# Optimization experiments

Measured on AMD Instinct MI355X. Metric: run time of the kernel, lower is better.

The kernel has to match this reference:

```python
import jax, jax.numpy as jnp
import numpy as np

OUTPUT_LEN = 128

def setup_inputs() -> dict:
    key = jax.random.key(0)
    k1, k2, k3 = jax.random.split(key, 3)
    B, D = 256, 1024
    scale = 1.0 / np.sqrt(D)
    x = jax.random.normal(k1, (B, D), dtype=jnp.float32)
    W = jax.random.normal(k2, (D, 3 * D), dtype=jnp.float32) * scale  # input kernel [d, 3d] (z|r|h)
    U = jax.random.normal(k3, (D, 3 * D), dtype=jnp.float32) * scale  # recurrent kernel [d, 3d]
    b = jnp.zeros((3 * D,), dtype=jnp.float32)
    return {"x": x, "W": W, "U": U, "b": b}

def _gru_cell(inp, h, W, U, b):
    # Classic GRU (reset_after=False), Keras gate order z, r, h and
    # update rule h_new = z * h + (1 - z) * hh.
    gx = inp @ W + b              # [B, 3d]
    gh = h @ U                    # [B, 3d]
    xz, xr, xh = jnp.split(gx, 3, axis=-1)
    hz, hr, hh_lin = jnp.split(gh, 3, axis=-1)
    z = jax.nn.sigmoid(xz + hz)
    r = jax.nn.sigmoid(xr + hr)
    hh = jnp.tanh(xh + r * hh_lin)
    return z * h + (1.0 - z) * hh

def reference(x, W, U, b):
    # x: [B, d] is the initial GRU state; the first step's input is zeros,
    # afterwards each step's output (== new state) is fed back as input.
    def step(carry, _):
        inp, h = carry
        new_h = _gru_cell(inp, h, W, U, b)
        return (new_h, new_h), new_h

    init = (jnp.zeros_like(x), x)
    _, outs = jax.lax.scan(step, init, None, length=OUTPUT_LEN)  # [T, B, d]
    return jnp.transpose(outs, (1, 0, 2))  # [B, T, d]
```

## Files before the change

### kernel.cpp

```cpp
#include <hip/hip_runtime.h>
#include <stdint.h>

#define B_ROWS 256
#define DDIM   1024
#define TSTEPS 128
#define THREE_D 3072

typedef short bf16x8 __attribute__((ext_vector_type(8)));
typedef float f32x4  __attribute__((ext_vector_type(4)));
typedef unsigned short u16x8 __attribute__((ext_vector_type(8)));

static __device__ __forceinline__ unsigned short f2bf(float f) {
    union { float f; uint32_t u; } v; v.f = f;
    uint32_t u = v.u;
    uint32_t r = u + 0x7FFFu + ((u >> 16) & 1u);
    return (unsigned short)(r >> 16);
}
static __device__ __forceinline__ float bf2f(unsigned short h) {
    union { uint32_t u; float f; } v; v.u = ((uint32_t)h) << 16; return v.f;
}

__global__ __launch_bounds__(256) void pack_kernel(
    const float* __restrict__ W, const float* __restrict__ U,
    unsigned short* __restrict__ phi, unsigned short* __restrict__ plo)
{
    int t = blockIdx.x * 256 + threadIdx.x;
    int lane  = t & 63;
    int ktile = (t >> 6) & 31;
    int ntile = t >> 11;
    int col = ntile * 16 + (lane & 15);
    int q = col >> 10;
    int d = col & 1023;
    int k8 = ktile * 32 + ((lane >> 4) << 3);

    u16x8 ohi, olo;
    #pragma unroll
    for (int j = 0; j < 8; ++j) {
        int k = k8 + j;
        const float* wr = W + (size_t)k * THREE_D;
        const float* ur = U + (size_t)k * THREE_D;
        float v;
        if (q == 0)      v = wr[d] + ur[d];
        else if (q == 1) v = wr[1024 + d] + ur[1024 + d];
        else if (q == 2) v = wr[2048 + d];
        else             v = ur[2048 + d];
        unsigned short hi = f2bf(v);
        ohi[j] = hi;
        olo[j] = f2bf(v - bf2f(hi));
    }
    size_t base = ((size_t)(ntile * 32 + ktile) * 64 + lane) * 8;
    *(u16x8*)(phi + base) = ohi;
    *(u16x8*)(plo + base) = olo;
}

__global__ __launch_bounds__(256) void gru_step0(
    const float* __restrict__ x, const float* __restrict__ U,
    const float* __restrict__ bias,
    float* __restrict__ out,
    unsigned short* __restrict__ hbh, unsigned short* __restrict__ hbl)
{
    __shared__ float xt[16][64];
    const int tid = threadIdx.x;
    const int c   = tid & 63;
    const int rg  = tid >> 6;
    const int dt  = blockIdx.x & 15;
    const int rt  = blockIdx.x >> 4;

    float acc[4][3];
    #pragma unroll
    for (int rr = 0; rr < 4; ++rr) { acc[rr][0] = 0.f; acc[rr][1] = 0.f; acc[rr][2] = 0.f; }

    for (int kc = 0; kc < 16; ++kc) {
        #pragma unroll
        for (int i = 0; i < 4; ++i) {
            int e = i * 256 + tid;
            int row = e >> 6, kk = e & 63;
            xt[row][kk] = x[(size_t)(rt * 16 + row) * DDIM + kc * 64 + kk];
        }
        __syncthreads();
        #pragma unroll 4
        for (int kk = 0; kk < 64; ++kk) {
            int k = kc * 64 + kk;
            const float* up = U + (size_t)k * THREE_D + dt * 64 + c;
            float uz = up[0], ur = up[1024], uh = up[2048];
            #pragma unroll
            for (int rr = 0; rr < 4; ++rr) {
                float xv = xt[rg * 4 + rr][kk];
                acc[rr][0] += xv * uz;
                acc[rr][1] += xv * ur;
                acc[rr][2] += xv * uh;
            }
        }
        __syncthreads();
    }

    int d = dt * 64 + c;
    #pragma unroll
    for (int rr = 0; rr < 4; ++rr) {
        int row = rt * 16 + rg * 4 + rr;
        float z  = 1.0f / (1.0f + __expf(-(acc[rr][0] + bias[d])));
        float r  = 1.0f / (1.0f + __expf(-(acc[rr][1] + bias[1024 + d])));
        float hh = tanhf(bias[2048 + d] + r * acc[rr][2]);
        float hp = x[(size_t)row * DDIM + d];
        float hn = z * hp + (1.0f - z) * hh;
        out[(size_t)row * (TSTEPS * DDIM) + d] = hn;
        unsigned short hi = f2bf(hn);
        size_t off = (size_t)row * DDIM + d;
        hbh[off] = hi;
        hbl[off] = f2bf(hn - bf2f(hi));
    }
}

__global__ __launch_bounds__(256) void gru_step(
    const unsigned short* __restrict__ phi,
    const unsigned short* __restrict__ plo,
    const unsigned short* __restrict__ hbh_in,
    const unsigned short* __restrict__ hbl_in,
    const float* __restrict__ bias,
    float* __restrict__ out,
    unsigned short* __restrict__ hbh_out,
    unsigned short* __restrict__ hbl_out,
    int t)
{
    __shared__ float gbuf[4][64][16];
    const int tid  = threadIdx.x;
    const int lane = tid & 63;
    const int q    = tid >> 6;
    const int dt   = blockIdx.x & 63;
    const int rt   = blockIdx.x >> 6;
    const int llow = lane & 15;
    const int lhi  = lane >> 4;

    f32x4 acc[4] = {f32x4{0,0,0,0}, f32x4{0,0,0,0}, f32x4{0,0,0,0}, f32x4{0,0,0,0}};

    const int ntile = q * 64 + dt;
    const unsigned short* bhp = phi + ((size_t)ntile * 2048 + lane) * 8;
    const unsigned short* blp = plo + ((size_t)ntile * 2048 + lane) * 8;
    const unsigned short* ahp = hbh_in + (size_t)(rt * 64 + llow) * DDIM + lhi * 8;
    const unsigned short* alp = hbl_in + (size_t)(rt * 64 + llow) * DDIM + lhi * 8;

    #pragma unroll 2
    for (int kt = 0; kt < 32; ++kt) {
        bf16x8 bh = *(const bf16x8*)(bhp + (size_t)kt * 512);
        bf16x8 bl = *(const bf16x8*)(blp + (size_t)kt * 512);
        const int koff = kt * 32;
        #pragma unroll
        for (int m = 0; m < 4; ++m) {
            bf16x8 ah = *(const bf16x8*)(ahp + (size_t)m * 16 * DDIM + koff);
            bf16x8 al = *(const bf16x8*)(alp + (size_t)m * 16 * DDIM + koff);
            acc[m] = __builtin_amdgcn_mfma_f32_16x16x32_bf16(ah, bh, acc[m], 0, 0, 0);
            acc[m] = __builtin_amdgcn_mfma_f32_16x16x32_bf16(al, bh, acc[m], 0, 0, 0);
            acc[m] = __builtin_amdgcn_mfma_f32_16x16x32_bf16(ah, bl, acc[m], 0, 0, 0);
        }
    }

    #pragma unroll
    for (int m = 0; m < 4; ++m) {
        #pragma unroll
        for (int r = 0; r < 4; ++r) {
            gbuf[q][m * 16 + lhi * 4 + r][llow] = acc[m][r];
        }
    }
    __syncthreads();

    #pragma unroll
    for (int i = 0; i < 4; ++i) {
        int e = tid + i * 256;
        int row = e >> 4, col = e & 15;
        int d = dt * 16 + col;
        int grow = rt * 64 + row;
        float gz = gbuf[0][row][col] + bias[d];
        float gr = gbuf[1][row][col] + bias[1024 + d];
        float gx = gbuf[2][row][col] + bias[2048 + d];
        float gu = gbuf[3][row][col];
        float z  = 1.0f / (1.0f + __expf(-gz));
        float r  = 1.0f / (1.0f + __expf(-gr));
        float hh = tanhf(gx + r * gu);
        size_t orow = (size_t)grow * (TSTEPS * DDIM);
        float hp = out[orow + (size_t)(t - 1) * DDIM + d];
        float hn = z * hp + (1.0f - z) * hh;
        out[orow + (size_t)t * DDIM + d] = hn;
        unsigned short hi = f2bf(hn);
        size_t hoff = (size_t)grow * DDIM + d;
        hbh_out[hoff] = hi;
        hbl_out[hoff] = f2bf(hn - bf2f(hi));
    }
}

extern "C" void kernel_launch(void* const* d_in, const int* in_sizes, int n_in,
                              void* d_out, int out_size, void* d_ws, size_t ws_size,
                              hipStream_t stream) {
    const float* x = (const float*)d_in[0];
    const float* W = (const float*)d_in[1];
    const float* U = (const float*)d_in[2];
    const float* b = (const float*)d_in[3];
    float* out = (float*)d_out;

    char* ws = (char*)d_ws;
    unsigned short* phi = (unsigned short*)ws;
    unsigned short* plo = (unsigned short*)(ws + (8u << 20));
    char* hbase = ws + (16u << 20);
    unsigned short* hbh[2] = { (unsigned short*)hbase,
                               (unsigned short*)(hbase + (512u << 10)) };
    unsigned short* hbl[2] = { (unsigned short*)(hbase + (1024u << 10)),
                               (unsigned short*)(hbase + (1536u << 10)) };

    hipLaunchKernelGGL(pack_kernel, dim3(2048), dim3(256), 0, stream, W, U, phi, plo);
    hipLaunchKernelGGL(gru_step0, dim3(256), dim3(256), 0, stream, x, U, b,
                       out, hbh[0], hbl[0]);

    for (int t = 1; t < TSTEPS; ++t) {
        int src = (t - 1) & 1;
        int dst = t & 1;
        hipLaunchKernelGGL(gru_step, dim3(256), dim3(256), 0, stream,
                           phi, plo, hbh[src], hbl[src], b,
                           out, hbh[dst], hbl[dst], t);
    }
}
```

Before: 4.675 ms.

## Split K across four wave groups per block and run step zero on MFMA

Result: slower. 6.600 ms (+41.2%).

```diff
diff --git a/kernel.cpp b/kernel.cpp
--- a/kernel.cpp
+++ b/kernel.cpp
@@ -5,6 +5,7 @@
 #define DDIM   1024
 #define TSTEPS 128
 #define THREE_D 3072
+#define OSTRIDE (TSTEPS * DDIM)
 
 typedef short bf16x8 __attribute__((ext_vector_type(8)));
 typedef float f32x4  __attribute__((ext_vector_type(4)));
@@ -51,6 +52,131 @@
     size_t base = ((size_t)(ntile * 32 + ktile) * 64 + lane) * 8;
     *(u16x8*)(phi + base) = ohi;
     *(u16x8*)(plo + base) = olo;
+}
+
+__global__ __launch_bounds__(256) void pack0_kernel(
+    const float* __restrict__ U,
+    unsigned short* __restrict__ phi, unsigned short* __restrict__ plo)
+{
+    int t = blockIdx.x * 256 + threadIdx.x;
+    int lane  = t & 63;
+    int ktile = (t >> 6) & 31;
+    int ntile = t >> 11;
+    int col = ntile * 16 + (lane & 15);
+    int q = col >> 10;
+    int d = col & 1023;
+    int k8 = ktile * 32 + ((lane >> 4) << 3);
+
+    u16x8 ohi, olo;
+    #pragma unroll
+    for (int j = 0; j < 8; ++j) {
+        int k = k8 + j;
+        const float* ur = U + (size_t)k * THREE_D;
+        float v;
+        if (q == 0)      v = ur[d];
+        else if (q == 1) v = ur[1024 + d];
+        else if (q == 2) v = 0.0f;
+        else             v = ur[2048 + d];
+        unsigned short hi = f2bf(v);
+        ohi[j] = hi;
+        olo[j] = f2bf(v - bf2f(hi));
+    }
+    size_t base = ((size_t)(ntile * 32 + ktile) * 64 + lane) * 8;
+    *(u16x8*)(phi + base) = ohi;
+    *(u16x8*)(plo + base) = olo;
+}
+
+__global__ __launch_bounds__(256) void init_x(
+    const float* __restrict__ x,
+    unsigned short* __restrict__ xh, unsigned short* __restrict__ xl)
+{
+    int i = blockIdx.x * 256 + threadIdx.x;
+    if (i < B_ROWS * DDIM) {
+        float v = x[i];
+        unsigned short h = f2bf(v);
+        xh[i] = h;
+        xl[i] = f2bf(v - bf2f(h));
+    }
+}
+
+__global__ __launch_bounds__(1024) void gru_step(
+    const unsigned short* __restrict__ phi,
+    const unsigned short* __restrict__ plo,
+    const unsigned short* __restrict__ hbh_in,
+    const unsigned short* __restrict__ hbl_in,
+    const float* __restrict__ bias,
+    const float* __restrict__ hprev, int hstride,
+    float* __restrict__ out_t,
+    unsigned short* __restrict__ hbh_out,
+    unsigned short* __restrict__ hbl_out)
+{
+    __shared__ float pbuf[4][64][17];
+    const int tid  = threadIdx.x;
+    const int w    = tid >> 6;
+    const int lane = tid & 63;
+    const int q    = w & 3;
+    const int kq   = w >> 2;
+    const int dt   = blockIdx.x & 63;
+    const int rt   = blockIdx.x >> 6;
+    const int llow = lane & 15;
+    const int lhi  = lane >> 4;
+
+    float* pf = &pbuf[0][0][0];
+    for (int i = tid; i < 4 * 64 * 17; i += 1024) pf[i] = 0.0f;
+    __syncthreads();
+
+    f32x4 acc[4] = {f32x4{0,0,0,0}, f32x4{0,0,0,0}, f32x4{0,0,0,0}, f32x4{0,0,0,0}};
+
+    const int ntile = q * 64 + dt;
+    const unsigned short* bhp = phi + (size_t)ntile * 16384 + (size_t)kq * 4096 + (size_t)lane * 8;
+    const unsigned short* blp = plo + (size_t)ntile * 16384 + (size_t)kq * 4096 + (size_t)lane * 8;
+    const size_t arow = (size_t)(rt * 64 + llow) * DDIM + kq * 256 + lhi * 8;
+    const unsigned short* ahp = hbh_in + arow;
+    const unsigned short* alp = hbl_in + arow;
+
+    #pragma unroll 2
+    for (int kt = 0; kt < 8; ++kt) {
+        bf16x8 bh = *(const bf16x8*)(bhp + kt * 512);
+        bf16x8 bl = *(const bf16x8*)(blp + kt * 512);
+        const int koff = kt * 32;
+        #pragma unroll
+        for (int m = 0; m < 4; ++m) {
+            bf16x8 ah = *(const bf16x8*)(ahp + m * 16 * DDIM + koff);
+            bf16x8 al = *(const bf16x8*)(alp + m * 16 * DDIM + koff);
+            acc[m] = __builtin_amdgcn_mfma_f32_16x16x32_bf16(ah, bh, acc[m], 0, 0, 0);
+            acc[m] = __builtin_amdgcn_mfma_f32_16x16x32_bf16(al, bh, acc[m], 0, 0, 0);
+            acc[m] = __builtin_amdgcn_mfma_f32_16x16x32_bf16(ah, bl, acc[m], 0, 0, 0);
+        }
+    }
+
+    #pragma unroll
+    for (int m = 0; m < 4; ++m) {
+        #pragma unroll
+        for (int r = 0; r < 4; ++r) {
+            atomicAdd(&pbuf[q][m * 16 + lhi * 4 + r][llow], acc[m][r]);
+        }
+    }
+    __syncthreads();
+
+    {
+        int row = tid >> 4, col = tid & 15;
+        int d = dt * 16 + col;
+        int grow = rt * 64 + row;
+        float gz = pbuf[0][row][col] + bias[d];
+        float gr = pbuf[1][row][col] + bias[1024 + d];
+        float gx = pbuf[2][row][col] + bias[2048 + d];
+        float gu = pbuf[3][row][col];
+        float z  = 1.0f / (1.0f + __expf(-gz));
+        float r  = 1.0f / (1.0f + __expf(-gr));
+        float hh = tanhf(gx + r * gu);
+        float hp = hprev[(size_t)grow * hstride + d];
+        float hn = z * hp + (1.0f - z) * hh;
+        out_t[(size_t)grow * OSTRIDE + d] = hn;
+        unsigned short hi = f2bf(hn);
+        size_t hoff = (size_t)grow * DDIM + d;
+        hbh_out[hoff] = hi;
+        hbl_out[hoff] = f2bf(hn - bf2f(hi));
+    }
 }
 
 __global__ __launch_bounds__(256) void gru_step0(
@@ -103,87 +229,11 @@
         float hh = tanhf(bias[2048 + d] + r * acc[rr][2]);
         float hp = x[(size_t)row * DDIM + d];
         float hn = z * hp + (1.0f - z) * hh;
-        out[(size_t)row * (TSTEPS * DDIM) + d] = hn;
+        out[(size_t)row * OSTRIDE + d] = hn;
         unsigned short hi = f2bf(hn);
         size_t off = (size_t)row * DDIM + d;
         hbh[off] = hi;
         hbl[off] = f2bf(hn - bf2f(hi));
-    }
-}
-
-__global__ __launch_bounds__(256) void gru_step(
-    const unsigned short* __restrict__ phi,
-    const unsigned short* __restrict__ plo,
-    const unsigned short* __restrict__ hbh_in,
-    const unsigned short* __restrict__ hbl_in,
-    const float* __restrict__ bias,
-    float* __restrict__ out,
-    unsigned short* __restrict__ hbh_out,
-    unsigned short* __restrict__ hbl_out,
-    int t)
-{
-    __shared__ float gbuf[4][64][16];
-    const int tid  = threadIdx.x;
-    const int lane = tid & 63;
-    const int q    = tid >> 6;
-    const int dt   = blockIdx.x & 63;
-    const int rt   = blockIdx.x >> 6;
-    const int llow = lane & 15;
-    const int lhi  = lane >> 4;
-
-    f32x4 acc[4] = {f32x4{0,0,0,0}, f32x4{0,0,0,0}, f32x4{0,0,0,0}, f32x4{0,0,0,0}};
-
-    const int ntile = q * 64 + dt;
-    const unsigned short* bhp = phi + ((size_t)ntile * 2048 + lane) * 8;
-    const unsigned short* blp = plo + ((size_t)ntile * 2048 + lane) * 8;
-    const unsigned short* ahp = hbh_in + (size_t)(rt * 64 + llow) * DDIM + lhi * 8;
-    const unsigned short* alp = hbl_in + (size_t)(rt * 64 + llow) * DDIM + lhi * 8;
-
-    #pragma unroll 2
-    for (int kt = 0; kt < 32; ++kt) {
-        bf16x8 bh = *(const bf16x8*)(bhp + (size_t)kt * 512);
-        bf16x8 bl = *(const bf16x8*)(blp + (size_t)kt * 512);
-        const int koff = kt * 32;
-        #pragma unroll
-        for (int m = 0; m < 4; ++m) {
-            bf16x8 ah = *(const bf16x8*)(ahp + (size_t)m * 16 * DDIM + koff);
-            bf16x8 al = *(const bf16x8*)(alp + (size_t)m * 16 * DDIM + koff);
-            acc[m] = __builtin_amdgcn_mfma_f32_16x16x32_bf16(ah, bh, acc[m], 0, 0, 0);
-            acc[m] = __builtin_amdgcn_mfma_f32_16x16x32_bf16(al, bh, acc[m], 0, 0, 0);
-            acc[m] = __builtin_amdgcn_mfma_f32_16x16x32_bf16(ah, bl, acc[m], 0, 0, 0);
-        }
-    }
-
-    #pragma unroll
-    for (int m = 0; m < 4; ++m) {
-        #pragma unroll
-        for (int r = 0; r < 4; ++r) {
-            gbuf[q][m * 16 + lhi * 4 + r][llow] = acc[m][r];
-        }
-    }
-    __syncthreads();
-
-    #pragma unroll
-    for (int i = 0; i < 4; ++i) {
-        int e = tid + i * 256;
-        int row = e >> 4, col = e & 15;
-        int d = dt * 16 + col;
-        int grow = rt * 64 + row;
-        float gz = gbuf[0][row][col] + bias[d];
-        float gr = gbuf[1][row][col] + bias[1024 + d];
-        float gx = gbuf[2][row][col] + bias[2048 + d];
-        float gu = gbuf[3][row][col];
-        float z  = 1.0f / (1.0f + __expf(-gz));
-        float r  = 1.0f / (1.0f + __expf(-gr));
-        float hh = tanhf(gx + r * gu);
-        size_t orow = (size_t)grow * (TSTEPS * DDIM);
-        float hp = out[orow + (size_t)(t - 1) * DDIM + d];
-        float hn = z * hp + (1.0f - z) * hh;
-        out[orow + (size_t)t * DDIM + d] = hn;
-        unsigned short hi = f2bf(hn);
-        size_t hoff = (size_t)grow * DDIM + d;
-        hbh_out[hoff] = hi;
-        hbl_out[hoff] = f2bf(hn - bf2f(hi));
     }
 }
 
@@ -197,23 +247,39 @@
     float* out = (float*)d_out;
 
     char* ws = (char*)d_ws;
-    unsigned short* phi = (unsigned short*)ws;
-    unsigned short* plo = (unsigned short*)(ws + (8u << 20));
+    unsigned short* p1h = (unsigned short*)ws;
+    unsigned short* p1l = (unsigned short*)(ws + (8u << 20));
     char* hbase = ws + (16u << 20);
     unsigned short* hbh[2] = { (unsigned short*)hbase,
                                (unsigned short*)(hbase + (512u << 10)) };
     unsigned short* hbl[2] = { (unsigned short*)(hbase + (1024u << 10)),
                                (unsigned short*)(hbase + (1536u << 10)) };
-
-    hipLaunchKernelGGL(pack_kernel, dim3(2048), dim3(256), 0, stream, W, U, phi, plo);
-    hipLaunchKernelGGL(gru_step0, dim3(256), dim3(256), 0, stream, x, U, b,
-                       out, hbh[0], hbl[0]);
+    unsigned short* p0h = (unsigned short*)(ws + (18u << 20));
+    unsigned short* p0l = (unsigned short*)(ws + (26u << 20));
+    const bool mfma_step0 = (ws_size >= (34ull << 20));
+
+    hipLaunchKernelGGL(pack_kernel, dim3(2048), dim3(256), 0, stream, W, U, p1h, p1l);
+
+    if (mfma_step0) {
+        hipLaunchKernelGGL(pack0_kernel, dim3(2048), dim3(256), 0, stream, U, p0h, p0l);
+        hipLaunchKernelGGL(init_x, dim3(1024), dim3(256), 0, stream, x, hbh[1], hbl[1]);
+        hipLaunchKernelGGL(gru_step, dim3(256), dim3(1024), 0, stream,
+                           p0h, p0l, hbh[1], hbl[1], b,
+                           x, DDIM,
+                           out,
+                           hbh[0], hbl[0]);
+    } else {
+        hipLaunchKernelGGL(gru_step0, dim3(256), dim3(256), 0, stream, x, U, b,
+                           out, hbh[0], hbl[0]);
+    }
 
     for (int t = 1; t < TSTEPS; ++t) {
         int src = (t - 1) & 1;
         int dst = t & 1;
-        hipLaunchKernelGGL(gru_step, dim3(256), dim3(256), 0, stream,
-                           phi, plo, hbh[src], hbl[src], b,
-                           out, hbh[dst], hbl[dst], t);
-    }
-}
+        hipLaunchKernelGGL(gru_step, dim3(256), dim3(1024), 0, stream,
+                           p1h, p1l, hbh[src], hbl[src], b,
+                           out + (size_t)(t - 1) * DDIM, OSTRIDE,
+                           out + (size_t)t * DDIM,
+                           hbh[dst], hbl[dst]);
+    }
+}
```

## Fuse all GRU steps into one persistent cooperative kernel with grid sync

Applied to the files above, without the earlier changes.

Result: slower. 18.39 ms (+293.3%).

```diff
diff --git a/kernel.cpp b/kernel.cpp
--- a/kernel.cpp
+++ b/kernel.cpp
@@ -1,10 +1,14 @@
 #include <hip/hip_runtime.h>
+#include <hip/hip_cooperative_groups.h>
 #include <stdint.h>
+
+namespace cg = cooperative_groups;
 
 #define B_ROWS 256
 #define DDIM   1024
 #define TSTEPS 128
 #define THREE_D 3072
+#define OSTRIDE (TSTEPS * DDIM)
 
 typedef short bf16x8 __attribute__((ext_vector_type(8)));
 typedef float f32x4  __attribute__((ext_vector_type(4)));
@@ -20,11 +24,11 @@
     union { uint32_t u; float f; } v; v.u = ((uint32_t)h) << 16; return v.f;
 }
 
-__global__ __launch_bounds__(256) void pack_kernel(
-    const float* __restrict__ W, const float* __restrict__ U,
-    unsigned short* __restrict__ phi, unsigned short* __restrict__ plo)
+static __device__ __forceinline__ void pack_item(
+    int t, const float* __restrict__ W, const float* __restrict__ U,
+    unsigned short* __restrict__ p1h, unsigned short* __restrict__ p1l,
+    unsigned short* __restrict__ p0h, unsigned short* __restrict__ p0l)
 {
-    int t = blockIdx.x * 256 + threadIdx.x;
     int lane  = t & 63;
     int ktile = (t >> 6) & 31;
     int ntile = t >> 11;
@@ -33,157 +37,147 @@
     int d = col & 1023;
     int k8 = ktile * 32 + ((lane >> 4) << 3);
 
-    u16x8 ohi, olo;
+    u16x8 o1h, o1l, o0h, o0l;
     #pragma unroll
     for (int j = 0; j < 8; ++j) {
         int k = k8 + j;
         const float* wr = W + (size_t)k * THREE_D;
         const float* ur = U + (size_t)k * THREE_D;
-        float v;
-        if (q == 0)      v = wr[d] + ur[d];
-        else if (q == 1) v = wr[1024 + d] + ur[1024 + d];
-        else if (q == 2) v = wr[2048 + d];
-        else             v = ur[2048 + d];
-        unsigned short hi = f2bf(v);
-        ohi[j] = hi;
-        olo[j] = f2bf(v - bf2f(hi));
+        float v1, v0;
+        if (q == 0)      { float u = ur[d];        v1 = wr[d] + u;        v0 = u; }
+        else if (q == 1) { float u = ur[1024 + d]; v1 = wr[1024 + d] + u; v0 = u; }
+        else if (q == 2) { v1 = wr[2048 + d]; v0 = 0.0f; }
+        else             { float u = ur[2048 + d]; v1 = u; v0 = u; }
+        unsigned short h1 = f2bf(v1);
+        o1h[j] = h1; o1l[j] = f2bf(v1 - bf2f(h1));
+        unsigned short h0 = f2bf(v0);
+        o0h[j] = h0; o0l[j] = f2bf(v0 - bf2f(h0));
     }
     size_t base = ((size_t)(ntile * 32 + ktile) * 64 + lane) * 8;
-    *(u16x8*)(phi + base) = ohi;
-    *(u16x8*)(plo + base) = olo;
-}
-
-__global__ __launch_bounds__(256) void gru_step0(
-    const float* __restrict__ x, const float* __restrict__ U,
-    const float* __restrict__ bias,
+    *(u16x8*)(p1h + base) = o1h;
+    *(u16x8*)(p1l + base) = o1l;
+    *(u16x8*)(p0h + base) = o0h;
+    *(u16x8*)(p0l + base) = o0l;
+}
+
+__global__ __launch_bounds__(1024) void gru_all(
+    const float* __restrict__ x, const float* __restrict__ W,
+    const float* __restrict__ U, const float* __restrict__ bias,
     float* __restrict__ out,
-    unsigned short* __restrict__ hbh, unsigned short* __restrict__ hbl)
+    unsigned short* __restrict__ p1h, unsigned short* __restrict__ p1l,
+    unsigned short* __restrict__ p0h, unsigned short* __restrict__ p0l,
+    unsigned short* __restrict__ h0h, unsigned short* __restrict__ h0l,
+    unsigned short* __restrict__ h1h, unsigned short* __restrict__ h1l)
 {
-    __shared__ float xt[16][64];
+    cg::grid_group grid = cg::this_grid();
+    __shared__ float pbuf[4][64][17];
+
     const int tid = threadIdx.x;
-    const int c   = tid & 63;
-    const int rg  = tid >> 6;
-    const int dt  = blockIdx.x & 15;
-    const int rt  = blockIdx.x >> 4;
-
-    float acc[4][3];
-    #pragma unroll
-    for (int rr = 0; rr < 4; ++rr) { acc[rr][0] = 0.f; acc[rr][1] = 0.f; acc[rr][2] = 0.f; }
-
-    for (int kc = 0; kc < 16; ++kc) {
+    const int blk = blockIdx.x;
+    const int dt  = blk & 63;
+    const int rt  = blk >> 6;
+
+    {
+        int gt = blk * 1024 + tid;
+        pack_item(gt,          W, U, p1h, p1l, p0h, p0l);
+        pack_item(gt + 262144, W, U, p1h, p1l, p0h, p0l);
+    }
+
+    const int row  = tid >> 4;
+    const int col  = tid & 15;
+    const int grow = rt * 64 + row;
+    const int d    = dt * 16 + col;
+    const size_t hoff = (size_t)grow * DDIM + d;
+
+    float hp = x[hoff];
+    {
+        unsigned short hi = f2bf(hp);
+        h0h[hoff] = hi;
+        h0l[hoff] = f2bf(hp - bf2f(hi));
+    }
+    const float bz  = bias[d];
+    const float br  = bias[1024 + d];
+    const float bhb = bias[2048 + d];
+    float* outp = out + (size_t)grow * OSTRIDE + d;
+
+    {
+        float* pf = &pbuf[0][0][0];
+        for (int i = tid; i < 4 * 64 * 17; i += 1024) pf[i] = 0.0f;
+    }
+
+    const int lane = tid & 63;
+    const int w    = tid >> 6;
+    const int q    = w & 3;
+    const int kh   = (w >> 2) & 1;
+    const int mh   = w >> 3;
+    const int llow = lane & 15;
+    const int lhi  = lane >> 4;
+
+    const int ntile = q * 64 + dt;
+    const size_t bbase = ((size_t)ntile * 32 + (size_t)kh * 16) * 512 + (size_t)lane * 8;
+    const size_t abase = (size_t)(rt * 64 + mh * 32 + llow) * DDIM + kh * 512 + lhi * 8;
+
+    const int prow0 = (mh * 2) * 16 + lhi * 4;
+    const int prow1 = (mh * 2 + 1) * 16 + lhi * 4;
+
+    __threadfence();
+    grid.sync();
+
+    for (int t = 0; t < TSTEPS; ++t) {
+        const unsigned short* bhp = ((t == 0) ? p0h : p1h) + bbase;
+        const unsigned short* blp = ((t == 0) ? p0l : p1l) + bbase;
+        const unsigned short* ahp = ((t & 1) ? h1h : h0h) + abase;
+        const unsigned short* alp = ((t & 1) ? h1l : h0l) + abase;
+        unsigned short* hoh = (t & 1) ? h0h : h1h;
+        unsigned short* hol = (t & 1) ? h0l : h1l;
+
+        f32x4 acc0 = {0.f, 0.f, 0.f, 0.f};
+        f32x4 acc1 = {0.f, 0.f, 0.f, 0.f};
+
+        #pragma unroll 2
+        for (int kt = 0; kt < 16; ++kt) {
+            bf16x8 bh  = *(const bf16x8*)(bhp + kt * 512);
+            bf16x8 bl  = *(const bf16x8*)(blp + kt * 512);
+            bf16x8 a0h = *(const bf16x8*)(ahp + kt * 32);
+            bf16x8 a0l = *(const bf16x8*)(alp + kt * 32);
+            bf16x8 a1h = *(const bf16x8*)(ahp + 16 * DDIM + kt * 32);
+            bf16x8 a1l = *(const bf16x8*)(alp + 16 * DDIM + kt * 32);
+            acc0 = __builtin_amdgcn_mfma_f32_16x16x32_bf16(a0h, bh, acc0, 0, 0, 0);
+            acc0 = __builtin_amdgcn_mfma_f32_16x16x32_bf16(a0l, bh, acc0, 0, 0, 0);
+            acc0 = __builtin_amdgcn_mfma_f32_16x16x32_bf16(a0h, bl, acc0, 0, 0, 0);
+            acc1 = __builtin_amdgcn_mfma_f32_16x16x32_bf16(a1h, bh, acc1, 0, 0, 0);
+            acc1 = __builtin_amdgcn_mfma_f32_16x16x32_bf16(a1l, bh, acc1, 0, 0, 0);
+            acc1 = __builtin_amdgcn_mfma_f32_16x16x32_bf16(a1h, bl, acc1, 0, 0, 0);
+        }
+
         #pragma unroll
-        for (int i = 0; i < 4; ++i) {
-            int e = i * 256 + tid;
-            int row = e >> 6, kk = e & 63;
-            xt[row][kk] = x[(size_t)(rt * 16 + row) * DDIM + kc * 64 + kk];
+        for (int r = 0; r < 4; ++r) {
+            atomicAdd(&pbuf[q][prow0 + r][llow], acc0[r]);
+            atomicAdd(&pbuf[q][prow1 + r][llow], acc1[r]);
         }
         __syncthreads();
-        #pragma unroll 4
-        for (int kk = 0; kk < 64; ++kk) {
-            int k = kc * 64 + kk;
-            const float* up = U + (size_t)k * THREE_D + dt * 64 + c;
-            float uz = up[0], ur = up[1024], uh = up[2048];
-            #pragma unroll
-            for (int rr = 0; rr < 4; ++rr) {
-                float xv = xt[rg * 4 + rr][kk];
-                acc[rr][0] += xv * uz;
-                acc[rr][1] += xv * ur;
-                acc[rr][2] += xv * uh;
-            }
+
+        float gz = pbuf[0][row][col] + bz;
+        float gr = pbuf[1][row][col] + br;
+        float gx = pbuf[2][row][col] + bhb;
+        float gu = pbuf[3][row][col];
+        float z  = 1.0f / (1.0f + __expf(-gz));
+        float r_ = 1.0f / (1.0f + __expf(-gr));
+        float hh = tanhf(gx + r_ * gu);
+        float hn = z * hp + (1.0f - z) * hh;
+        hp = hn;
+        outp[t * DDIM] = hn;
+        unsigned short hi = f2bf(hn);
+        hoh[hoff] = hi;
+        hol[hoff] = f2bf(hn - bf2f(hi));
+        __syncthreads();
+
+        {
+            float* pf = &pbuf[0][0][0];
+            for (int i = tid; i < 4 * 64 * 17; i += 1024) pf[i] = 0.0f;
         }
-        __syncthreads();
-    }
-
-    int d = dt * 64 + c;
-    #pragma unroll
-    for (int rr = 0; rr < 4; ++rr) {
-        int row = rt * 16 + rg * 4 + rr;
-        float z  = 1.0f / (1.0f + __expf(-(acc[rr][0] + bias[d])));
-        float r  = 1.0f / (1.0f + __expf(-(acc[rr][1] + bias[1024 + d])));
-        float hh = tanhf(bias[2048 + d] + r * acc[rr][2]);
-        float hp = x[(size_t)row * DDIM + d];
-        float hn = z * hp + (1.0f - z) * hh;
-        out[(size_t)row * (TSTEPS * DDIM) + d] = hn;
-        unsigned short hi = f2bf(hn);
-        size_t off = (size_t)row * DDIM + d;
-        hbh[off] = hi;
-        hbl[off] = f2bf(hn - bf2f(hi));
-    }
-}
-
-__global__ __launch_bounds__(256) void gru_step(
-    const unsigned short* __restrict__ phi,
-    const unsigned short* __restrict__ plo,
-    const unsigned short* __restrict__ hbh_in,
-    const unsigned short* __restrict__ hbl_in,
-    const float* __restrict__ bias,
-    float* __restrict__ out,
-    unsigned short* __restrict__ hbh_out,
-    unsigned short* __restrict__ hbl_out,
-    int t)
-{
-    __shared__ float gbuf[4][64][16];
-    const int tid  = threadIdx.x;
-    const int lane = tid & 63;
-    const int q    = tid >> 6;
-    const int dt   = blockIdx.x & 63;
-    const int rt   = blockIdx.x >> 6;
-    const int llow = lane & 15;
-    const int lhi  = lane >> 4;
-
-    f32x4 acc[4] = {f32x4{0,0,0,0}, f32x4{0,0,0,0}, f32x4{0,0,0,0}, f32x4{0,0,0,0}};
-
-    const int ntile = q * 64 + dt;
-    const unsigned short* bhp = phi + ((size_t)ntile * 2048 + lane) * 8;
-    const unsigned short* blp = plo + ((size_t)ntile * 2048 + lane) * 8;
-    const unsigned short* ahp = hbh_in + (size_t)(rt * 64 + llow) * DDIM + lhi * 8;
-    const unsigned short* alp = hbl_in + (size_t)(rt * 64 + llow) * DDIM + lhi * 8;
-
-    #pragma unroll 2
-    for (int kt = 0; kt < 32; ++kt) {
-        bf16x8 bh = *(const bf16x8*)(bhp + (size_t)kt * 512);
-        bf16x8 bl = *(const bf16x8*)(blp + (size_t)kt * 512);
-        const int koff = kt * 32;
-        #pragma unroll
-        for (int m = 0; m < 4; ++m) {
-            bf16x8 ah = *(const bf16x8*)(ahp + (size_t)m * 16 * DDIM + koff);
-            bf16x8 al = *(const bf16x8*)(alp + (size_t)m * 16 * DDIM + koff);
-            acc[m] = __builtin_amdgcn_mfma_f32_16x16x32_bf16(ah, bh, acc[m], 0, 0, 0);
-            acc[m] = __builtin_amdgcn_mfma_f32_16x16x32_bf16(al, bh, acc[m], 0, 0, 0);
-            acc[m] = __builtin_amdgcn_mfma_f32_16x16x32_bf16(ah, bl, acc[m], 0, 0, 0);
-        }
-    }
-
-    #pragma unroll
-    for (int m = 0; m < 4; ++m) {
-        #pragma unroll
-        for (int r = 0; r < 4; ++r) {
-            gbuf[q][m * 16 + lhi * 4 + r][llow] = acc[m][r];
-        }
-    }
-    __syncthreads();
-
-    #pragma unroll
-    for (int i = 0; i < 4; ++i) {
-        int e = tid + i * 256;
-        int row = e >> 4, col = e & 15;
-        int d = dt * 16 + col;
-        int grow = rt * 64 + row;
-        float gz = gbuf[0][row][col] + bias[d];
-        float gr = gbuf[1][row][col] + bias[1024 + d];
-        float gx = gbuf[2][row][col] + bias[2048 + d];
-        float gu = gbuf[3][row][col];
-        float z  = 1.0f / (1.0f + __expf(-gz));
-        float r  = 1.0f / (1.0f + __expf(-gr));
-        float hh = tanhf(gx + r * gu);
-        size_t orow = (size_t)grow * (TSTEPS * DDIM);
-        float hp = out[orow + (size_t)(t - 1) * DDIM + d];
-        float hn = z * hp + (1.0f - z) * hh;
-        out[orow + (size_t)t * DDIM + d] = hn;
-        unsigned short hi = f2bf(hn);
-        size_t hoff = (size_t)grow * DDIM + d;
-        hbh_out[hoff] = hi;
-        hbl_out[hoff] = f2bf(hn - bf2f(hi));
+        __threadfence();
+        grid.sync();
     }
 }
 
@@ -197,23 +191,21 @@
     float* out = (float*)d_out;
 
     char* ws = (char*)d_ws;
-    unsigned short* phi = (unsigned short*)ws;
-    unsigned short* plo = (unsigned short*)(ws + (8u << 20));
-    char* hbase = ws + (16u << 20);
-    unsigned short* hbh[2] = { (unsigned short*)hbase,
-                               (unsigned short*)(hbase + (512u << 10)) };
-    unsigned short* hbl[2] = { (unsigned short*)(hbase + (1024u << 10)),
-                               (unsigned short*)(hbase + (1536u << 10)) };
-
-    hipLaunchKernelGGL(pack_kernel, dim3(2048), dim3(256), 0, stream, W, U, phi, plo);
-    hipLaunchKernelGGL(gru_step0, dim3(256), dim3(256), 0, stream, x, U, b,
-                       out, hbh[0], hbl[0]);
-
-    for (int t = 1; t < TSTEPS; ++t) {
-        int src = (t - 1) & 1;
-        int dst = t & 1;
-        hipLaunchKernelGGL(gru_step, dim3(256), dim3(256), 0, stream,
-                           phi, plo, hbh[src], hbl[src], b,
-                           out, hbh[dst], hbl[dst], t);
-    }
-}
+    unsigned short* p1h = (unsigned short*)ws;
+    unsigned short* p1l = (unsigned short*)(ws + (8u << 20));
+    unsigned short* p0h = (unsigned short*)(ws + (16u << 20));
+    unsigned short* p0l = (unsigned short*)(ws + (24u << 20));
+    char* hbase = ws + (32u << 20);
+    unsigned short* h0h = (unsigned short*)hbase;
+    unsigned short* h0l = (unsigned short*)(hbase + (512u << 10));
+    unsigned short* h1h = (unsigned short*)(hbase + (1024u << 10));
+    unsigned short* h1l = (unsigned short*)(hbase + (1536u << 10));
+
+    void* args[] = {
+        (void*)&x, (void*)&W, (void*)&U, (void*)&b, (void*)&out,
+        (void*)&p1h, (void*)&p1l, (void*)&p0h, (void*)&p0l,
+        (void*)&h0h, (void*)&h0l, (void*)&h1h, (void*)&h1l
+    };
+    hipLaunchCooperativeKernel((const void*)gru_all, dim3(256), dim3(1024),
+                               args, 0, stream);
+}
```
